# Kernel tuning notes

Measured on AMD Instinct MI355X. Metric: run time of the kernel, lower is better.

## Reference

```python
import jax, jax.numpy as jnp
import numpy as np

N = 100000      # nodes
E = 1600000     # edges
D = 128         # embedding_size (num_heads=1)
L = 4           # num_layers
NEG_SLOPE_ATT = 0.2    # GATConv attention LeakyReLU
NEG_SLOPE_ACT = 0.01   # nn.LeakyReLU default
LN_EPS = 1e-5


def leaky(x, s):
    return jnp.where(x > 0, x, s * x)


def layer_norm(x, gamma, beta):
    mu = jnp.mean(x, axis=-1, keepdims=True)
    var = jnp.mean(jnp.square(x - mu), axis=-1, keepdims=True)
    return (x - mu) * jax.lax.rsqrt(var + LN_EPS) * gamma + beta


def gat_conv(x, src, dst, W, a_src, a_dst, b):
    # PyG GATConv, heads=1, add_self_loops=False, no edge features
    h = x @ W                                  # [N, D]
    alpha_src = h @ a_src                      # [N]
    alpha_dst = h @ a_dst                      # [N]
    e = leaky(alpha_src[src] + alpha_dst[dst], NEG_SLOPE_ATT)   # [E]
    # softmax over incoming edges of each destination node
    m = jax.ops.segment_max(e, dst, num_segments=N)             # [N]
    ex = jnp.exp(e - m[dst])
    denom = jax.ops.segment_sum(ex, dst, num_segments=N)        # [N]
    alpha = ex / (denom[dst] + 1e-16)                           # [E]
    out = jax.ops.segment_sum(alpha[:, None] * h[src], dst, num_segments=N)
    return out + b


def setup_inputs() -> dict:
    key = jax.random.key(0)
    ks = jax.random.split(key, 12)
    x = jax.random.normal(ks[0], (N, D), dtype=jnp.float32)
    edge_index = jax.random.randint(ks[1], (2, E), 0, N, dtype=jnp.int32)
    s = 0.05
    return {
        "x": x,
        "edge_index": edge_index,
        "W_in": jax.random.normal(ks[2], (D, D), dtype=jnp.float32) * s,
        "b_in": jnp.zeros((D,), dtype=jnp.float32),
        "Wl": jax.random.normal(ks[3], (L, D, D), dtype=jnp.float32) * s,
        "att_src": jax.random.normal(ks[4], (L, D), dtype=jnp.float32) * s,
        "att_dst": jax.random.normal(ks[5], (L, D), dtype=jnp.float32) * s,
        "bias_l": jnp.zeros((L, D), dtype=jnp.float32),
        "gamma": jnp.ones((L, D), dtype=jnp.float32),
        "beta": jnp.zeros((L, D), dtype=jnp.float32),
    }


def reference(x, edge_index, W_in, b_in, Wl, att_src, att_dst, bias_l, gamma, beta):
    src, dst = edge_index[0], edge_index[1]
    h = leaky(x @ W_in + b_in, NEG_SLOPE_ACT)
    for i in range(L):
        h = gat_conv(h, src, dst, Wl[i], att_src[i], att_dst[i], bias_l[i])
        h = layer_norm(h, gamma[i], beta[i])
        h = leaky(h, NEG_SLOPE_ACT)
        # dropout p=0.3 is identity in eval mode; pooling undefined in source -> identity
    return h
```

## Files before the change

kernel.cpp:

```cpp
#include <hip/hip_runtime.h>
#include <hip/hip_fp16.h>
#include <math.h>

#define NN 100000
#define EE 1600000
#define DD 128
#define NBUCK 196
#define NBLKP 196
#define EPB 8192

typedef _Float16 f16;
typedef f16 f16x8 __attribute__((ext_vector_type(8)));
typedef float f32x4 __attribute__((ext_vector_type(4)));

#define LDA 136
#define WCHUNKS 2304

__global__ __launch_bounds__(256) void part_hist_k(const int* __restrict__ dst, int* __restrict__ bcnt) {
    __shared__ int lc[NBUCK];
    int t = threadIdx.x, blk = blockIdx.x;
    if (t < NBUCK) lc[t] = 0;
    __syncthreads();
    int e0 = blk * EPB;
    for (int i = t; i < EPB; i += 256) {
        int e = e0 + i;
        if (e < EE) atomicAdd(&lc[dst[e] >> 9], 1);
    }
    __syncthreads();
    if (t < NBUCK) bcnt[t * NBLKP + blk] = lc[t];
}

__global__ __launch_bounds__(256) void scanBB_k(const int* __restrict__ bcnt, int* __restrict__ ebase,
                                                int* __restrict__ btot) {
    __shared__ int sh[256];
    int t = threadIdx.x, b = blockIdx.x;
    int c = (t < NBLKP) ? bcnt[b * NBLKP + t] : 0;
    sh[t] = c;
    __syncthreads();
    for (int off = 1; off < 256; off <<= 1) {
        int v = (t >= off) ? sh[t - off] : 0;
        __syncthreads();
        sh[t] += v;
        __syncthreads();
    }
    if (t < NBLKP) ebase[b * NBLKP + t] = sh[t] - c;
    if (t == 255) btot[b] = sh[255];
}

__global__ __launch_bounds__(256) void scanBT_k(const int* __restrict__ btot, int* __restrict__ bstart,
                                                int* __restrict__ offsets) {
    __shared__ int sh[256];
    int t = threadIdx.x;
    int c = (t < NBUCK) ? btot[t] : 0;
    sh[t] = c;
    __syncthreads();
    for (int off = 1; off < 256; off <<= 1) {
        int v = (t >= off) ? sh[t - off] : 0;
        __syncthreads();
        sh[t] += v;
        __syncthreads();
    }
    if (t < NBUCK) bstart[t] = sh[t] - c;
    if (t == 0) { bstart[NBUCK] = EE; offsets[NN] = EE; }
}

__global__ __launch_bounds__(256) void part_k(const int* __restrict__ src, const int* __restrict__ dst,
                                              const int* __restrict__ bstart, const int* __restrict__ ebase,
                                              int2* __restrict__ ebuf) {
    __shared__ int cur[NBUCK];
    int t = threadIdx.x, blk = blockIdx.x;
    if (t < NBUCK) cur[t] = bstart[t] + ebase[t * NBLKP + blk];
    __syncthreads();
    int e0 = blk * EPB;
    for (int i = t; i < EPB; i += 256) {
        int e = e0 + i;
        if (e < EE) {
            int s = src[e], d = dst[e];
            int p = atomicAdd(&cur[d >> 9], 1);
            ebuf[p] = make_int2(s, d);
        }
    }
}

__global__ __launch_bounds__(512) void bucket_sort_k(const int2* __restrict__ ebuf,
                                                     const int* __restrict__ bstart,
                                                     int* __restrict__ offsets,
                                                     int* __restrict__ ssrc,
                                                     int* __restrict__ sdst) {
    __shared__ int sh[512];
    __shared__ int cur[512];
    int t = threadIdx.x, b = blockIdx.x;
    int d0 = b << 9;
    int beg = bstart[b], end = bstart[b + 1];

    cur[t] = 0;
    __syncthreads();
    for (int e = beg + t; e < end; e += 512) atomicAdd(&cur[ebuf[e].y - d0], 1);
    __syncthreads();
    int c = cur[t];
    sh[t] = c;
    __syncthreads();
    for (int off = 1; off < 512; off <<= 1) {
        int v = (t >= off) ? sh[t - off] : 0;
        __syncthreads();
        sh[t] += v;
        __syncthreads();
    }
    int excl = sh[t] - c;
    if (d0 + t < NN) offsets[d0 + t] = beg + excl;
    cur[t] = beg + excl;
    __syncthreads();
    for (int e = beg + t; e < end; e += 512) {
        int2 ed = ebuf[e];
        int p = atomicAdd(&cur[ed.y - d0], 1);
        ssrc[p] = ed.x;
        sdst[p] = ed.y;
    }
}

__global__ __launch_bounds__(256) void wprep_k(const float* __restrict__ W_in,
                                               const float* __restrict__ Wl,
                                               const float* __restrict__ att_src,
                                               const float* __restrict__ att_dst,
                                               f16* __restrict__ Wt,
                                               float* __restrict__ wav) {
    int m = blockIdx.x;
    const float* src = (m == 0) ? W_in : (Wl + (size_t)(m - 1) * DD * DD);
    f16* dst = Wt + (size_t)m * (WCHUNKS * 8);
    for (int q = 0; q < 64; ++q) {
        int idx = q * 256 + threadIdx.x;
        int k = idx >> 7, n = idx & 127;
        dst[n * LDA + k] = (f16)src[idx];
    }
    if (m >= 1) {
        int t = threadIdx.x;
        const float* av = (t < 128) ? (att_src + (size_t)(m - 1) * DD)
                                    : (att_dst + (size_t)(m - 1) * DD);
        int k = t & 127;
        float s = 0.f;
        for (int n = 0; n < 128; ++n) s += src[k * 128 + n] * av[n];
        wav[(size_t)(m - 1) * 256 + (t >> 7) * 128 + k] = s;
    }
}

template <int FUSED>
__global__ __launch_bounds__(256, 2) void gemm_k(const void* __restrict__ Xv,
                                                 const f16* __restrict__ Wt0,
                                                 const f16* __restrict__ Wt1,
                                                 const float* __restrict__ bias,
                                                 const float* __restrict__ wa_s,
                                                 const float* __restrict__ wa_d,
                                                 __half* __restrict__ Yh,
                                                 float* __restrict__ alpha_src,
                                                 float* __restrict__ alpha_dst) {
    __shared__ __align__(16) f16 sW[WCHUNKS * 8];
    __shared__ __align__(16) f16 sOut[4][32][LDA];
    int t = threadIdx.x;
    int w = t >> 6, lane = t & 63;
    int cl = lane & 15, qw = lane >> 4;
    int row0 = blockIdx.x * 128;

    f16x8 a[2][4];
    if (FUSED) {
        const float* X = (const float*)Xv;
#pragma unroll
        for (int rf = 0; rf < 2; ++rf) {
            int row = row0 + w * 32 + rf * 16 + cl;
            row = row < NN ? row : NN - 1;
            const float* p = X + (size_t)row * DD;
#pragma unroll
            for (int ks = 0; ks < 4; ++ks) {
                float4 u0 = *(const float4*)(p + ks * 32 + qw * 8);
                float4 u1 = *(const float4*)(p + ks * 32 + qw * 8 + 4);
                f16x8 v;
                v[0] = (f16)u0.x; v[1] = (f16)u0.y; v[2] = (f16)u0.z; v[3] = (f16)u0.w;
                v[4] = (f16)u1.x; v[5] = (f16)u1.y; v[6] = (f16)u1.z; v[7] = (f16)u1.w;
                a[rf][ks] = v;
            }
        }
    } else {
        const f16* X = (const f16*)Xv;
#pragma unroll
        for (int rf = 0; rf < 2; ++rf) {
            int row = row0 + w * 32 + rf * 16 + cl;
            row = row < NN ? row : NN - 1;
            const f16* p = X + (size_t)row * DD;
#pragma unroll
            for (int ks = 0; ks < 4; ++ks)
                a[rf][ks] = *(const f16x8*)(p + ks * 32 + qw * 8);
        }
    }

    {
        const uint4* wsrc = (const uint4*)Wt0;
        uint4* wdst = (uint4*)sW;
#pragma unroll
        for (int it = 0; it < 9; ++it) wdst[it * 256 + t] = wsrc[it * 256 + t];
    }
    __syncthreads();

    f32x4 acc[2][8] = {};
#pragma unroll
    for (int ks = 0; ks < 4; ++ks) {
        int koff = ks * 32 + qw * 8;
#pragma unroll
        for (int nf = 0; nf < 8; ++nf) {
            f16x8 bh = *(const f16x8*)(sW + (nf * 16 + cl) * LDA + koff);
            acc[0][nf] = __builtin_amdgcn_mfma_f32_16x16x32_f16(a[0][ks], bh, acc[0][nf], 0, 0, 0);
            acc[1][nf] = __builtin_amdgcn_mfma_f32_16x16x32_f16(a[1][ks], bh, acc[1][nf], 0, 0, 0);
        }
    }

    if (FUSED) {
        __syncthreads();
        {
            const uint4* wsrc = (const uint4*)Wt1;
            uint4* wdst = (uint4*)sW;
#pragma unroll
            for (int it = 0; it < 9; ++it) wdst[it * 256 + t] = wsrc[it * 256 + t];
        }
        float bc[8];
#pragma unroll
        for (int nf = 0; nf < 8; ++nf) bc[nf] = bias[nf * 16 + cl];
#pragma unroll
        for (int rf = 0; rf < 2; ++rf)
#pragma unroll
            for (int i = 0; i < 4; ++i)
#pragma unroll
                for (int nf = 0; nf < 8; ++nf) {
                    float v = acc[rf][nf][i] + bc[nf];
                    v = v > 0.f ? v : 0.01f * v;
                    sOut[w][rf * 16 + qw * 4 + i][nf * 16 + cl] = (f16)v;
                }
        __syncthreads();
#pragma unroll
        for (int rf = 0; rf < 2; ++rf)
#pragma unroll
            for (int ks = 0; ks < 4; ++ks)
                a[rf][ks] = *(const f16x8*)&sOut[w][rf * 16 + cl][ks * 32 + qw * 8];
#pragma unroll
        for (int rf = 0; rf < 2; ++rf)
#pragma unroll
            for (int nf = 0; nf < 8; ++nf)
                acc[rf][nf] = (f32x4){0.f, 0.f, 0.f, 0.f};
#pragma unroll
        for (int ks = 0; ks < 4; ++ks) {
            int koff = ks * 32 + qw * 8;
#pragma unroll
            for (int nf = 0; nf < 8; ++nf) {
                f16x8 bh = *(const f16x8*)(sW + (nf * 16 + cl) * LDA + koff);
                acc[0][nf] = __builtin_amdgcn_mfma_f32_16x16x32_f16(a[0][ks], bh, acc[0][nf], 0, 0, 0);
                acc[1][nf] = __builtin_amdgcn_mfma_f32_16x16x32_f16(a[1][ks], bh, acc[1][nf], 0, 0, 0);
            }
        }
    }

#pragma unroll
    for (int rf = 0; rf < 2; ++rf) {
        float pa = 0.f, pb = 0.f;
#pragma unroll
        for (int ks = 0; ks < 4; ++ks) {
            const float* ps = wa_s + ks * 32 + qw * 8;
            const float* pd = wa_d + ks * 32 + qw * 8;
            float4 s0 = *(const float4*)ps, s1 = *(const float4*)(ps + 4);
            float4 d0 = *(const float4*)pd, d1 = *(const float4*)(pd + 4);
            float sv[8] = {s0.x, s0.y, s0.z, s0.w, s1.x, s1.y, s1.z, s1.w};
            float dv[8] = {d0.x, d0.y, d0.z, d0.w, d1.x, d1.y, d1.z, d1.w};
#pragma unroll
            for (int e = 0; e < 8; ++e) {
                float f = (float)a[rf][ks][e];
                pa = fmaf(f, sv[e], pa);
                pb = fmaf(f, dv[e], pb);
            }
        }
        pa += __shfl_xor(pa, 16); pa += __shfl_xor(pa, 32);
        pb += __shfl_xor(pb, 16); pb += __shfl_xor(pb, 32);
        if (qw == 0) {
            int row = row0 + w * 32 + rf * 16 + cl;
            if (row < NN) {
                alpha_src[row] = pa;
                alpha_dst[row] = pb;
            }
        }
    }

#pragma unroll
    for (int rf = 0; rf < 2; ++rf)
#pragma unroll
        for (int i = 0; i < 4; ++i)
#pragma unroll
            for (int nf = 0; nf < 8; ++nf)
                sOut[w][rf * 16 + qw * 4 + i][nf * 16 + cl] = (f16)acc[rf][nf][i];
#pragma unroll
    for (int p = 0; p < 8; ++p) {
        int rl = p * 4 + qw;
        uint4 v = *(const uint4*)&sOut[w][rl][cl * 8];
        int row = row0 + w * 32 + rl;
        if (row < NN) *(uint4*)(Yh + (size_t)row * DD + cl * 8) = v;
    }
}

__global__ __launch_bounds__(256) void edgew_k(const int* __restrict__ ssrc,
                                               const int* __restrict__ sdst,
                                               const float* __restrict__ alpha_src,
                                               const float* __restrict__ alpha_dst,
                                               int2* __restrict__ epk) {
    int j = blockIdx.x * 256 + threadIdx.x;
    if (j < EE) {
        int s = ssrc[j];
        float e = alpha_src[s] + alpha_dst[sdst[j]];
        e = e > 0.f ? e : 0.2f * e;
        epk[j] = make_int2(s, __float_as_int(__expf(e)));
    } else if (j < EE + 16) {
        epk[j] = make_int2(0, 0);
    }
}

template <int HOUT>
__global__ __launch_bounds__(256) void agg_k(const __half* __restrict__ tmp,
                                             const int2* __restrict__ epk,
                                             const int* __restrict__ offsets,
                                             const float* __restrict__ bias,
                                             const float* __restrict__ gamma,
                                             const float* __restrict__ beta,
                                             void* __restrict__ outv) {
    int wid = (blockIdx.x * 256 + threadIdx.x) >> 6;
    wid = __builtin_amdgcn_readfirstlane(wid);
    int lane = threadIdx.x & 63;
    int beg = __builtin_amdgcn_readfirstlane(offsets[wid]);
    int end = __builtin_amdgcn_readfirstlane(offsets[wid + 1]);

    const __half2* tmp2 = (const __half2*)tmp;
    float ax0 = 0.f, ay0 = 0.f, ax1 = 0.f, ay1 = 0.f, dsum = 0.f;

    for (int j = (beg & ~1); j < end; j += 16) {
        int4 q[8];
#pragma unroll
        for (int k = 0; k < 8; ++k) q[k] = *(const int4*)(epk + j + 2 * k);
        __half2 h[16];
#pragma unroll
        for (int k = 0; k < 8; ++k) {
            h[2 * k]     = tmp2[(size_t)q[k].x * 64 + lane];
            h[2 * k + 1] = tmp2[(size_t)q[k].z * 64 + lane];
        }
#pragma unroll
        for (int k = 0; k < 8; ++k) {
            int e0 = j + 2 * k, e1 = e0 + 1;
            bool v0 = (k == 0) ? (e0 >= beg && e0 < end) : (e0 < end);
            bool v1 = (e1 < end);
            float w0 = v0 ? __int_as_float(q[k].y) : 0.f;
            float w1 = v1 ? __int_as_float(q[k].w) : 0.f;
            dsum += w0 + w1;
            ax0 = fmaf(w0, __half2float(h[2 * k].x), ax0);
            ay0 = fmaf(w0, __half2float(h[2 * k].y), ay0);
            ax1 = fmaf(w1, __half2float(h[2 * k + 1].x), ax1);
            ay1 = fmaf(w1, __half2float(h[2 * k + 1].y), ay1);
        }
    }

    float inv = 1.0f / (dsum + 1e-16f);

    float ax = (ax0 + ax1) * inv + bias[2 * lane];
    float ay = (ay0 + ay1) * inv + bias[2 * lane + 1];

    float s1 = ax + ay;
#pragma unroll
    for (int off = 32; off >= 1; off >>= 1) s1 += __shfl_xor(s1, off);
    float mu = s1 * (1.0f / 128.0f);
    float dx = ax - mu, dy = ay - mu;
    float s2 = dx * dx + dy * dy;
#pragma unroll
    for (int off = 32; off >= 1; off >>= 1) s2 += __shfl_xor(s2, off);
    float rstd = rsqrtf(s2 * (1.0f / 128.0f) + 1e-5f);

    float yx = dx * rstd * gamma[2 * lane] + beta[2 * lane];
    float yy = dy * rstd * gamma[2 * lane + 1] + beta[2 * lane + 1];
    yx = yx > 0.f ? yx : 0.01f * yx;
    yy = yy > 0.f ? yy : 0.01f * yy;
    if (HOUT) {
        ((__half2*)outv)[(size_t)wid * 64 + lane] = __floats2half2_rn(yx, yy);
    } else {
        ((float2*)outv)[(size_t)wid * 64 + lane] = make_float2(yx, yy);
    }
}

extern "C" void kernel_launch(void* const* d_in, const int* in_sizes, int n_in,
                              void* d_out, int out_size, void* d_ws, size_t ws_size,
                              hipStream_t stream) {
    const float* x       = (const float*)d_in[0];
    const int*   ei      = (const int*)d_in[1];
    const float* W_in    = (const float*)d_in[2];
    const float* b_in    = (const float*)d_in[3];
    const float* Wl      = (const float*)d_in[4];
    const float* att_src = (const float*)d_in[5];
    const float* att_dst = (const float*)d_in[6];
    const float* bias_l  = (const float*)d_in[7];
    const float* gamma   = (const float*)d_in[8];
    const float* beta    = (const float*)d_in[9];
    float* out = (float*)d_out;

    char* ws = (char*)d_ws;
    __half* tmp      = (__half*)ws; ws += (size_t)NN * DD * 2;
    float* alpha_src = (float*)ws;  ws += (size_t)NN * 4;
    float* alpha_dst = (float*)ws;  ws += (size_t)NN * 4;
    int*   offsets   = (int*)ws;    ws += (size_t)(NN + 4) * 4;
    int*   ssrc      = (int*)ws;    ws += (size_t)EE * 4;
    int*   sdst      = (int*)ws;    ws += (size_t)EE * 4;
    int2*  ebuf      = (int2*)ws;   ws += (size_t)(EE + 16) * 8;
    int*   bcnt      = (int*)ws;    ws += (size_t)NBUCK * NBLKP * 4;
    int*   ebase     = (int*)ws;    ws += (size_t)NBUCK * NBLKP * 4;
    int*   btot      = (int*)ws;    ws += (size_t)(NBUCK + 4) * 4;
    int*   bstart    = (int*)ws;    ws += (size_t)(NBUCK + 4) * 4;
    f16*   Wt        = (f16*)ws;    ws += (size_t)5 * WCHUNKS * 16;
    float* wav       = (float*)ws;  ws += (size_t)4 * 256 * 4;
    int2* epk = ebuf;

    __half* hbuf = (__half*)d_out;

    const int* esrc = ei;
    const int* edst = ei + EE;

    part_hist_k<<<NBLKP, 256, 0, stream>>>(edst, bcnt);
    scanBB_k<<<NBUCK, 256, 0, stream>>>(bcnt, ebase, btot);
    scanBT_k<<<1, 256, 0, stream>>>(btot, bstart, offsets);
    part_k<<<NBLKP, 256, 0, stream>>>(esrc, edst, bstart, ebase, ebuf);
    bucket_sort_k<<<NBUCK, 512, 0, stream>>>(ebuf, bstart, offsets, ssrc, sdst);
    wprep_k<<<5, 256, 0, stream>>>(W_in, Wl, att_src, att_dst, Wt, wav);

    const int gg = (NN + 127) / 128;
    const int eg = (EE + 16 + 255) / 256;

    gemm_k<1><<<gg, 256, 0, stream>>>(x, Wt, Wt + (size_t)1 * (WCHUNKS * 8), b_in,
                                      wav, wav + 128, tmp, alpha_src, alpha_dst);
    edgew_k<<<eg, 256, 0, stream>>>(ssrc, sdst, alpha_src, alpha_dst, epk);
    agg_k<1><<<NN / 4, 256, 0, stream>>>(tmp, epk, offsets, bias_l, gamma, beta, (void*)hbuf);

    for (int i = 1; i < 4; i++) {
        gemm_k<0><<<gg, 256, 0, stream>>>(hbuf, Wt + (size_t)(i + 1) * (WCHUNKS * 8), nullptr, nullptr,
                                          wav + (size_t)i * 256, wav + (size_t)i * 256 + 128,
                                          tmp, alpha_src, alpha_dst);
        edgew_k<<<eg, 256, 0, stream>>>(ssrc, sdst, alpha_src, alpha_dst, epk);
        if (i < 3) {
            agg_k<1><<<NN / 4, 256, 0, stream>>>(tmp, epk, offsets,
                                                 bias_l + (size_t)i * DD, gamma + (size_t)i * DD,
                                                 beta + (size_t)i * DD, (void*)hbuf);
        } else {
            agg_k<0><<<NN / 4, 256, 0, stream>>>(tmp, epk, offsets,
                                                 bias_l + (size_t)i * DD, gamma + (size_t)i * DD,
                                                 beta + (size_t)i * DD, (void*)out);
        }
    }
}
```

Before: 547.2 us.

## Fuse edge-weight computation into aggregation and use buffer loads for gathers

Removes the per-layer edgew_k kernel and computes the attention weight exp(leaky(alpha_src[s]+alpha_dst[d])) inside agg_k, using the fact that every edge of a wave shares one destination. This drops the sdst array and the packed epk buffer, cutting edge-array traffic and a kernel launch per layer. The neighbour feature gather now uses raw buffer loads with a scalar offset per edge. In exchange, each aggregation wave does a random alpha_src gather and an exp per edge, the edge loop is aligned to groups of 4, and the padding tail of ssrc is zeroed.

```diff
diff --git a/kernel.cpp b/kernel.cpp
--- a/kernel.cpp
+++ b/kernel.cpp
@@ -12,6 +12,10 @@
 typedef _Float16 f16;
 typedef f16 f16x8 __attribute__((ext_vector_type(8)));
 typedef float f32x4 __attribute__((ext_vector_type(4)));
+typedef int int32x4 __attribute__((ext_vector_type(4)));
+
+__device__ float llvm_amdgcn_raw_buffer_load_fp32(int32x4 srsrc, int voffset, int soffset,
+                                                  int aux) __asm("llvm.amdgcn.raw.buffer.load.f32");
 
 #define LDA 136
 #define WCHUNKS 2304
@@ -85,14 +89,15 @@
 __global__ __launch_bounds__(512) void bucket_sort_k(const int2* __restrict__ ebuf,
                                                      const int* __restrict__ bstart,
                                                      int* __restrict__ offsets,
-                                                     int* __restrict__ ssrc,
-                                                     int* __restrict__ sdst) {
+                                                     int* __restrict__ ssrc) {
     __shared__ int sh[512];
     __shared__ int cur[512];
     int t = threadIdx.x, b = blockIdx.x;
     int d0 = b << 9;
     int beg = bstart[b], end = bstart[b + 1];
 
+    if (b == 0 && t < 16) ssrc[EE + t] = 0;
+
     cur[t] = 0;
     __syncthreads();
     for (int e = beg + t; e < end; e += 512) atomicAdd(&cur[ebuf[e].y - d0], 1);
@@ -114,7 +119,6 @@
         int2 ed = ebuf[e];
         int p = atomicAdd(&cur[ed.y - d0], 1);
         ssrc[p] = ed.x;
-        sdst[p] = ed.y;
     }
 }
 
@@ -300,26 +304,12 @@
     }
 }
 
-__global__ __launch_bounds__(256) void edgew_k(const int* __restrict__ ssrc,
-                                               const int* __restrict__ sdst,
-                                               const float* __restrict__ alpha_src,
-                                               const float* __restrict__ alpha_dst,
-                                               int2* __restrict__ epk) {
-    int j = blockIdx.x * 256 + threadIdx.x;
-    if (j < EE) {
-        int s = ssrc[j];
-        float e = alpha_src[s] + alpha_dst[sdst[j]];
-        e = e > 0.f ? e : 0.2f * e;
-        epk[j] = make_int2(s, __float_as_int(__expf(e)));
-    } else if (j < EE + 16) {
-        epk[j] = make_int2(0, 0);
-    }
-}
-
 template <int HOUT>
 __global__ __launch_bounds__(256) void agg_k(const __half* __restrict__ tmp,
-                                             const int2* __restrict__ epk,
+                                             const int* __restrict__ ssrc,
                                              const int* __restrict__ offsets,
+                                             const float* __restrict__ alpha_src,
+                                             const float* __restrict__ alpha_dst,
                                              const float* __restrict__ bias,
                                              const float* __restrict__ gamma,
                                              const float* __restrict__ beta,
@@ -329,32 +319,55 @@
     int lane = threadIdx.x & 63;
     int beg = __builtin_amdgcn_readfirstlane(offsets[wid]);
     int end = __builtin_amdgcn_readfirstlane(offsets[wid + 1]);
-
-    const __half2* tmp2 = (const __half2*)tmp;
+    float adst = alpha_dst[wid];
+
+    int32x4 rsrc;
+    {
+        unsigned long long b = (unsigned long long)(uintptr_t)tmp;
+        rsrc.x = (int)(b & 0xffffffffull);
+        rsrc.y = (int)(b >> 32);
+        rsrc.z = NN * 256;
+        rsrc.w = 0x00020000;
+    }
+    int voff = lane << 2;
+
     float ax0 = 0.f, ay0 = 0.f, ax1 = 0.f, ay1 = 0.f, dsum = 0.f;
 
-    for (int j = (beg & ~1); j < end; j += 16) {
-        int4 q[8];
-#pragma unroll
-        for (int k = 0; k < 8; ++k) q[k] = *(const int4*)(epk + j + 2 * k);
-        __half2 h[16];
-#pragma unroll
-        for (int k = 0; k < 8; ++k) {
-            h[2 * k]     = tmp2[(size_t)q[k].x * 64 + lane];
-            h[2 * k + 1] = tmp2[(size_t)q[k].z * 64 + lane];
-        }
-#pragma unroll
-        for (int k = 0; k < 8; ++k) {
-            int e0 = j + 2 * k, e1 = e0 + 1;
-            bool v0 = (k == 0) ? (e0 >= beg && e0 < end) : (e0 < end);
-            bool v1 = (e1 < end);
-            float w0 = v0 ? __int_as_float(q[k].y) : 0.f;
-            float w1 = v1 ? __int_as_float(q[k].w) : 0.f;
-            dsum += w0 + w1;
-            ax0 = fmaf(w0, __half2float(h[2 * k].x), ax0);
-            ay0 = fmaf(w0, __half2float(h[2 * k].y), ay0);
-            ax1 = fmaf(w1, __half2float(h[2 * k + 1].x), ax1);
-            ay1 = fmaf(w1, __half2float(h[2 * k + 1].y), ay1);
+    for (int j = (beg & ~3); j < end; j += 16) {
+        int4 sq[4];
+#pragma unroll
+        for (int k = 0; k < 4; ++k) sq[k] = *(const int4*)(ssrc + j + 4 * k);
+        int sv[16];
+#pragma unroll
+        for (int k = 0; k < 4; ++k) {
+            sv[4 * k] = sq[k].x; sv[4 * k + 1] = sq[k].y;
+            sv[4 * k + 2] = sq[k].z; sv[4 * k + 3] = sq[k].w;
+        }
+        float g[16];
+#pragma unroll
+        for (int k = 0; k < 16; ++k)
+            g[k] = llvm_amdgcn_raw_buffer_load_fp32(rsrc, voff, sv[k] << 8, 0);
+        float w[16];
+#pragma unroll
+        for (int k = 0; k < 16; ++k) {
+            float e = alpha_src[sv[k]] + adst;
+            e = e > 0.f ? e : 0.2f * e;
+            float ww = __expf(e);
+            int ei = j + k;
+            w[k] = (ei >= beg && ei < end) ? ww : 0.f;
+            dsum += w[k];
+        }
+#pragma unroll
+        for (int k = 0; k < 16; ++k) {
+            union { float f; __half2 h; } u;
+            u.f = g[k];
+            if (k & 1) {
+                ax1 = fmaf(w[k], __half2float(u.h.x), ax1);
+                ay1 = fmaf(w[k], __half2float(u.h.y), ay1);
+            } else {
+                ax0 = fmaf(w[k], __half2float(u.h.x), ax0);
+                ay0 = fmaf(w[k], __half2float(u.h.y), ay0);
+            }
         }
     }
 
@@ -404,16 +417,14 @@
     float* alpha_src = (float*)ws;  ws += (size_t)NN * 4;
     float* alpha_dst = (float*)ws;  ws += (size_t)NN * 4;
     int*   offsets   = (int*)ws;    ws += (size_t)(NN + 4) * 4;
-    int*   ssrc      = (int*)ws;    ws += (size_t)EE * 4;
-    int*   sdst      = (int*)ws;    ws += (size_t)EE * 4;
-    int2*  ebuf      = (int2*)ws;   ws += (size_t)(EE + 16) * 8;
+    int*   ssrc      = (int*)ws;    ws += (size_t)(EE + 16) * 4;
+    int2*  ebuf      = (int2*)ws;   ws += (size_t)EE * 8;
     int*   bcnt      = (int*)ws;    ws += (size_t)NBUCK * NBLKP * 4;
     int*   ebase     = (int*)ws;    ws += (size_t)NBUCK * NBLKP * 4;
     int*   btot      = (int*)ws;    ws += (size_t)(NBUCK + 4) * 4;
     int*   bstart    = (int*)ws;    ws += (size_t)(NBUCK + 4) * 4;
     f16*   Wt        = (f16*)ws;    ws += (size_t)5 * WCHUNKS * 16;
     float* wav       = (float*)ws;  ws += (size_t)4 * 256 * 4;
-    int2* epk = ebuf;
 
     __half* hbuf = (__half*)d_out;
 
@@ -424,28 +435,26 @@
     scanBB_k<<<NBUCK, 256, 0, stream>>>(bcnt, ebase, btot);
     scanBT_k<<<1, 256, 0, stream>>>(btot, bstart, offsets);
     part_k<<<NBLKP, 256, 0, stream>>>(esrc, edst, bstart, ebase, ebuf);
-    bucket_sort_k<<<NBUCK, 512, 0, stream>>>(ebuf, bstart, offsets, ssrc, sdst);
+    bucket_sort_k<<<NBUCK, 512, 0, stream>>>(ebuf, bstart, offsets, ssrc);
     wprep_k<<<5, 256, 0, stream>>>(W_in, Wl, att_src, att_dst, Wt, wav);
 
     const int gg = (NN + 127) / 128;
-    const int eg = (EE + 16 + 255) / 256;
 
     gemm_k<1><<<gg, 256, 0, stream>>>(x, Wt, Wt + (size_t)1 * (WCHUNKS * 8), b_in,
                                       wav, wav + 128, tmp, alpha_src, alpha_dst);
-    edgew_k<<<eg, 256, 0, stream>>>(ssrc, sdst, alpha_src, alpha_dst, epk);
-    agg_k<1><<<NN / 4, 256, 0, stream>>>(tmp, epk, offsets, bias_l, gamma, beta, (void*)hbuf);
+    agg_k<1><<<NN / 4, 256, 0, stream>>>(tmp, ssrc, offsets, alpha_src, alpha_dst,
+                                         bias_l, gamma, beta, (void*)hbuf);
 
     for (int i = 1; i < 4; i++) {
         gemm_k<0><<<gg, 256, 0, stream>>>(hbuf, Wt + (size_t)(i + 1) * (WCHUNKS * 8), nullptr, nullptr,
                                           wav + (size_t)i * 256, wav + (size_t)i * 256 + 128,
                                           tmp, alpha_src, alpha_dst);
-        edgew_k<<<eg, 256, 0, stream>>>(ssrc, sdst, alpha_src, alpha_dst, epk);
         if (i < 3) {
-            agg_k<1><<<NN / 4, 256, 0, stream>>>(tmp, epk, offsets,
+            agg_k<1><<<NN / 4, 256, 0, stream>>>(tmp, ssrc, offsets, alpha_src, alpha_dst,
                                                  bias_l + (size_t)i * DD, gamma + (size_t)i * DD,
                                                  beta + (size_t)i * DD, (void*)hbuf);
         } else {
-            agg_k<0><<<NN / 4, 256, 0, stream>>>(tmp, epk, offsets,
+            agg_k<0><<<NN / 4, 256, 0, stream>>>(tmp, ssrc, offsets, alpha_src, alpha_dst,
                                                  bias_l + (size_t)i * DD, gamma + (size_t)i * DD,
                                                  beta + (size_t)i * DD, (void*)out);
         }
```

Result: slower. 572.3 us (+4.6%).
